# Kernel tuning notes

Measured on AMD Instinct MI355X. Metric: run time of the kernel, lower is better.

Reference implementation:

```python
import jax, jax.numpy as jnp
import numpy as np

N_NODES = 200000
N_EDGES = 600000
FP = 128


def _gru_cell(x, h, wih, whh, bih, bhh):
    # torch.nn.GRUCell: gates ordered (r, z, n)
    gi = x @ wih.T + bih
    gh = h @ whh.T + bhh
    ir, iz, inn = jnp.split(gi, 3, axis=-1)
    hr, hz, hn = jnp.split(gh, 3, axis=-1)
    r = jax.nn.sigmoid(ir + hr)
    z = jax.nn.sigmoid(iz + hz)
    n = jnp.tanh(inn + r * hn)
    return (1.0 - z) * n + z * h


def _layer(x, dst, step, aw, ab, tw, tb, wih, whh, bih, bhh):
    n_nodes = x.shape[0]
    x_i = x[dst]  # [E, F] gather of target-node features
    if step == 0:
        h_s = jnp.broadcast_to(jnp.sum(x_i, axis=-1, keepdims=True), x_i.shape)
    else:
        h_s = x_i
    esv = jax.nn.leaky_relu(jnp.concatenate([h_s, x_i], axis=-1) @ aw.T + ab)  # [E,1]
    asv = jax.nn.softmax(esv, axis=-1)  # size-1 softmax -> ones (faithful)
    cs = jax.nn.elu(asv * (h_s @ tw.T + tb))  # dropout is identity at eval
    m = _gru_cell(cs, h_s, wih, whh, bih, bhh)  # per-edge GRU update [E,F]
    return jax.ops.segment_sum(m, dst, num_segments=n_nodes)  # scatter-add aggregate


def setup_inputs() -> dict:
    key = jax.random.key(0)
    ks = jax.random.split(key, 20)
    s = 1.0 / np.sqrt(FP)
    inp = {
        "x": jax.random.normal(ks[0], (N_NODES, FP), dtype=jnp.float32),
        "edge_index": jax.random.randint(ks[1], (2, N_EDGES), 0, N_NODES, dtype=jnp.int64),
    }
    i = 2
    for l in range(2):
        inp[f"align_w{l}"] = jax.random.uniform(ks[i], (1, 2 * FP), jnp.float32, -s, s); i += 1
        inp[f"align_b{l}"] = jax.random.uniform(ks[i], (1,), jnp.float32, -s, s); i += 1
        inp[f"attend_w{l}"] = jax.random.uniform(ks[i], (FP, FP), jnp.float32, -s, s); i += 1
        inp[f"attend_b{l}"] = jax.random.uniform(ks[i], (FP,), jnp.float32, -s, s); i += 1
        inp[f"wih{l}"] = jax.random.uniform(ks[i], (3 * FP, FP), jnp.float32, -s, s); i += 1
        inp[f"whh{l}"] = jax.random.uniform(ks[i], (3 * FP, FP), jnp.float32, -s, s); i += 1
        inp[f"bih{l}"] = jax.random.uniform(ks[i], (3 * FP,), jnp.float32, -s, s); i += 1
        inp[f"bhh{l}"] = jax.random.uniform(ks[i], (3 * FP,), jnp.float32, -s, s); i += 1
    return inp


def reference(x, edge_index,
              align_w0, align_b0, attend_w0, attend_b0, wih0, whh0, bih0, bhh0,
              align_w1, align_b1, attend_w1, attend_b1, wih1, whh1, bih1, bhh1):
    dst = edge_index[1]
    x = _layer(x, dst, 0, align_w0, align_b0, attend_w0, attend_b0, wih0, whh0, bih0, bhh0)
    x = _layer(x, dst, 1, align_w1, align_b1, attend_w1, attend_b1, wih1, whh1, bih1, bhh1)
    return x
```

## Files before the change

kernel.cpp:

```cpp
#include <hip/hip_runtime.h>
#include <cmath>

#define NN 200000
#define NE 600000

typedef __bf16 bf16x8 __attribute__((ext_vector_type(8)));
typedef float f32x16 __attribute__((ext_vector_type(16)));

#define LOG2E 1.44269504088896340736f
__device__ __forceinline__ float fexp2(float x) { return __builtin_amdgcn_exp2f(x); }
__device__ __forceinline__ float frcp(float x) { return __builtin_amdgcn_rcpf(x); }
__device__ __forceinline__ float sigm(float v) { return frcp(1.0f + fexp2(-LOG2E * v)); }
__device__ __forceinline__ float ftanh(float v) {
  float t = fexp2(-2.0f * LOG2E * fabsf(v));
  float r = (1.0f - t) * frcp(1.0f + t);
  return __builtin_copysignf(r, v);
}
__device__ __forceinline__ float eluf(float v) { return v > 0.0f ? v : fexp2(LOG2E * v) - 1.0f; }

__device__ __forceinline__ unsigned short bfr(float f) {
  unsigned u = __float_as_uint(f);
  u += 0x7FFFu + ((u >> 16) & 1u);
  return (unsigned short)(u >> 16);
}
__device__ __forceinline__ void bsplit(float v, unsigned short& hi, unsigned short& lo) {
  unsigned short h = bfr(v);
  float hf = __uint_as_float(((unsigned)h) << 16);
  hi = h;
  lo = bfr(v - hf);
}


__global__ __launch_bounds__(256) void hist_kernel(const int* __restrict__ dst,
                                                   int* __restrict__ deg) {
  int e = blockIdx.x * 256 + threadIdx.x;
  if (e < NE) atomicAdd(&deg[dst[e]], 1);
}

__global__ __launch_bounds__(256) void prep_kernel(const float* __restrict__ attw0,
                                                   const float* __restrict__ whh0,
                                                   float* __restrict__ rwt0,
                                                   float* __restrict__ rwh0) {
  int gw = blockIdx.x * 4 + (threadIdx.x >> 6);
  int lane = threadIdx.x & 63;
  const float* row = (gw < 128) ? (attw0 + (size_t)gw * 128)
                                : (whh0 + (size_t)(gw - 128) * 128);
  float2 v = ((const float2*)row)[lane];
  float a = v.x + v.y;
#pragma unroll
  for (int o = 1; o < 64; o <<= 1) a += __shfl_xor(a, o, 64);
  if (lane == 0) {
    if (gw < 128) rwt0[gw] = a;
    else rwh0[gw - 128] = a;
  }
}

__global__ __launch_bounds__(256) void pack_kernel(
    const float* __restrict__ wih0, const float* __restrict__ tw1,
    const float* __restrict__ wih1, const float* __restrict__ whh1,
    unsigned short* __restrict__ w0ph, unsigned short* __restrict__ w0pl,
    unsigned short* __restrict__ w1ph, unsigned short* __restrict__ w1pl,
    unsigned short* __restrict__ w2ph, unsigned short* __restrict__ w2pl) {
  int g = blockIdx.x * 256 + threadIdx.x;
  if (g >= 20480) return;
  unsigned short *PH, *PL;
  const float* row;
  int l;
  if (g < 6144) { l = g; PH = w0ph; PL = w0pl; }
  else if (g < 8192) { l = g - 6144; PH = w1ph; PL = w1pl; }
  else { l = g - 8192; PH = w2ph; PL = w2pl; }
  int lane = l & 63, ks = (l >> 6) & 7, nt = l >> 9;
  int n = nt * 32 + (lane & 31);
  int k0 = ks * 16 + (lane >> 5) * 8;
  if (g < 6144) row = wih0 + n * 128;
  else if (g < 8192) row = tw1 + n * 128;
  else row = (n < 384) ? wih1 + n * 128 : whh1 + (n - 384) * 128;
  unsigned uh[4], ul[4];
#pragma unroll
  for (int p = 0; p < 4; p++) {
    unsigned short ah, al, bh, bl;
    bsplit(row[k0 + 2 * p], ah, al);
    bsplit(row[k0 + 2 * p + 1], bh, bl);
    uh[p] = (unsigned)ah | ((unsigned)bh << 16);
    ul[p] = (unsigned)al | ((unsigned)bl << 16);
  }
  *(uint4*)&PH[l * 8] = make_uint4(uh[0], uh[1], uh[2], uh[3]);
  *(uint4*)&PL[l * 8] = make_uint4(ul[0], ul[1], ul[2], ul[3]);
}

#define MFMA3(accv, ah, al, bh, bl)                                          \
  accv = __builtin_amdgcn_mfma_f32_32x32x16_bf16(ah, bh, accv, 0, 0, 0);     \
  accv = __builtin_amdgcn_mfma_f32_32x32x16_bf16(ah, bl, accv, 0, 0, 0);     \
  accv = __builtin_amdgcn_mfma_f32_32x32x16_bf16(al, bh, accv, 0, 0, 0);

__global__ __launch_bounds__(512, 4) void layer0_kernel(
    const float* __restrict__ x, const float* __restrict__ tb0,
    const unsigned short* __restrict__ w0ph, const unsigned short* __restrict__ w0pl,
    const float* __restrict__ bih0, const float* __restrict__ bhh0,
    const float* __restrict__ rwt0, const float* __restrict__ rwh0,
    const int* __restrict__ deg,
    unsigned short* __restrict__ x1h, unsigned short* __restrict__ x1l) {
  __shared__ float s_lds[64];
  __shared__ float deg_lds[64];
  __shared__ unsigned short csh[8192];
  __shared__ unsigned short csl[8192];

  const int tid = threadIdx.x;
  const int lane = tid & 63;
  const int wv = tid >> 6;
  const int mg = wv & 1;
  const int cb = wv >> 1;
  const int n0 = blockIdx.x * 64;

  if (tid < 64) deg_lds[tid] = (float)deg[n0 + tid];

  {
    int m = tid >> 3, c = (tid & 7) * 16;
    const float4* xr = (const float4*)(x + (size_t)(n0 + m) * 128 + c);
    float a = 0.f;
#pragma unroll
    for (int q = 0; q < 4; q++) { float4 v = xr[q]; a += v.x + v.y + v.z + v.w; }
#pragma unroll
    for (int o = 1; o < 8; o <<= 1) a += __shfl_xor(a, o, 64);
    if ((tid & 7) == 0) s_lds[m] = a;
  }
  __syncthreads();

  {
    int m = lane, c = wv;
    float s = s_lds[m];
    int kb = c * 16;
    int fb = (((m >> 5) * 8 + c) * 64 + (m & 31)) * 8;
#pragma unroll
    for (int u = 0; u < 2; u++) {
      unsigned uh[4], ul[4];
#pragma unroll
      for (int p = 0; p < 4; p++) {
        int k = kb + u * 8 + p * 2;
        unsigned short h0, l0, h1, l1;
        bsplit(eluf(fmaf(s, rwt0[k], tb0[k])), h0, l0);
        bsplit(eluf(fmaf(s, rwt0[k + 1], tb0[k + 1])), h1, l1);
        uh[p] = (unsigned)h0 | ((unsigned)h1 << 16);
        ul[p] = (unsigned)l0 | ((unsigned)l1 << 16);
      }
      *(uint4*)&csh[fb + u * 256] = make_uint4(uh[0], uh[1], uh[2], uh[3]);
      *(uint4*)&csl[fb + u * 256] = make_uint4(ul[0], ul[1], ul[2], ul[3]);
    }
  }
  __syncthreads();

  f32x16 acc[3] = {};
#pragma unroll
  for (int ks = 0; ks < 8; ks++) {
    bf16x8 ah = *(const bf16x8*)&csh[((mg * 8 + ks) * 64 + lane) * 8];
    bf16x8 al = *(const bf16x8*)&csl[((mg * 8 + ks) * 64 + lane) * 8];
#pragma unroll
    for (int g = 0; g < 3; g++) {
      int nt = g * 4 + cb;
      size_t base = (size_t)((nt * 8 + ks) * 64 + lane) * 8;
      bf16x8 bh = *(const bf16x8*)&w0ph[base];
      bf16x8 bl = *(const bf16x8*)&w0pl[base];
      MFMA3(acc[g], ah, al, bh, bl);
    }
  }

  const int jc = cb * 32 + (lane & 31);
  float bir = bih0[jc], biz = bih0[jc + 128], bin_ = bih0[jc + 256];
  float bhr = bhh0[jc], bhz = bhh0[jc + 128], bhn = bhh0[jc + 256];
  float rwr = rwh0[jc], rwz = rwh0[jc + 128], rwn = rwh0[jc + 256];
  const size_t tbase = (size_t)blockIdx.x * 8192;
  const int fj = ((mg * 8 + (cb * 2 + ((lane >> 4) & 1))) * 64 + ((lane >> 3) & 1) * 32) * 8 +
                 (lane & 7);
#pragma unroll
  for (int reg = 0; reg < 16; reg++) {
    int crow = (reg & 3) + 8 * (reg >> 2) + 4 * (lane >> 5);
    int m = mg * 32 + crow;
    float s = s_lds[m];
    float dd = deg_lds[m];
    float r = sigm(acc[0][reg] + bir + fmaf(s, rwr, bhr));
    float z = sigm(acc[1][reg] + biz + fmaf(s, rwz, bhz));
    float nn2 = ftanh(fmaf(r, fmaf(s, rwn, bhn), acc[2][reg] + bin_));
    float v = dd * ((1.f - z) * nn2 + z * s);
    unsigned short vh, vl;
    bsplit(v, vh, vl);
    unsigned pv = (unsigned)vh | ((unsigned)vl << 16);
    unsigned pu = __shfl_xor(pv, 1, 64);
    if ((lane & 1) == 0) {
      size_t f = tbase + fj + crow * 8;
      *(unsigned*)&x1h[f] = (pv & 0xFFFFu) | (pu << 16);
      *(unsigned*)&x1l[f] = (pv >> 16) | (pu & 0xFFFF0000u);
    }
  }
}

__global__ __launch_bounds__(512, 4) void layer1_kernel(
    const unsigned short* __restrict__ x1h, const unsigned short* __restrict__ x1l,
    const float* __restrict__ tb1,
    const unsigned short* __restrict__ w1ph, const unsigned short* __restrict__ w1pl,
    const unsigned short* __restrict__ w2ph, const unsigned short* __restrict__ w2pl,
    const float* __restrict__ bih1, const float* __restrict__ bhh1,
    const int* __restrict__ deg, float* __restrict__ out) {
  __shared__ unsigned short cfh[8192];
  __shared__ unsigned short cfl[8192];
  __shared__ float deg_lds[64];

  const int tid = threadIdx.x;
  const int lane = tid & 63;
  const int wv = tid >> 6;
  const int mg = wv & 1;
  const int cb = wv >> 1;
  const int n0 = blockIdx.x * 64;
  const size_t tbase = (size_t)blockIdx.x * 8192;

  if (tid < 64) deg_lds[tid] = (float)deg[n0 + tid];

  f32x16 aA[4] = {};
#pragma unroll
  for (int ks = 0; ks < 8; ks++) {
    bf16x8 ah = *(const bf16x8*)&x1h[tbase + ((mg * 8 + ks) * 64 + lane) * 8];
    bf16x8 al = *(const bf16x8*)&x1l[tbase + ((mg * 8 + ks) * 64 + lane) * 8];
    {
      size_t base = (size_t)((cb * 8 + ks) * 64 + lane) * 8;
      bf16x8 bh = *(const bf16x8*)&w1ph[base];
      bf16x8 bl = *(const bf16x8*)&w1pl[base];
      MFMA3(aA[3], ah, al, bh, bl);
    }
#pragma unroll
    for (int g = 0; g < 3; g++) {
      int nt = 12 + g * 4 + cb;
      size_t base = (size_t)((nt * 8 + ks) * 64 + lane) * 8;
      bf16x8 bh = *(const bf16x8*)&w2ph[base];
      bf16x8 bl = *(const bf16x8*)&w2pl[base];
      MFMA3(aA[g], ah, al, bh, bl);
    }
  }

  {
    float tbj = tb1[cb * 32 + (lane & 31)];
    const int fj = ((mg * 8 + (cb * 2 + ((lane >> 4) & 1))) * 64 + ((lane >> 3) & 1) * 32) * 8 +
                   (lane & 7);
#pragma unroll
    for (int reg = 0; reg < 16; reg++) {
      int crow = (reg & 3) + 8 * (reg >> 2) + 4 * (lane >> 5);
      unsigned short vh, vl;
      bsplit(eluf(aA[3][reg] + tbj), vh, vl);
      unsigned pv = (unsigned)vh | ((unsigned)vl << 16);
      unsigned pu = __shfl_xor(pv, 1, 64);
      if ((lane & 1) == 0) {
        int f = fj + crow * 8;
        *(unsigned*)&cfh[f] = (pv & 0xFFFFu) | (pu << 16);
        *(unsigned*)&cfl[f] = (pv >> 16) | (pu & 0xFFFF0000u);
      }
    }
  }
  __syncthreads();

  f32x16 aB[1] = {};
#pragma unroll
  for (int ks = 0; ks < 8; ks++) {
    bf16x8 ch = *(const bf16x8*)&cfh[((mg * 8 + ks) * 64 + lane) * 8];
    bf16x8 cl = *(const bf16x8*)&cfl[((mg * 8 + ks) * 64 + lane) * 8];
#pragma unroll
    for (int g = 0; g < 3; g++) {
      int nt = g * 4 + cb;
      size_t base = (size_t)((nt * 8 + ks) * 64 + lane) * 8;
      bf16x8 bh = *(const bf16x8*)&w2ph[base];
      bf16x8 bl = *(const bf16x8*)&w2pl[base];
      if (g == 0) { MFMA3(aA[0], ch, cl, bh, bl); }
      else if (g == 1) { MFMA3(aA[1], ch, cl, bh, bl); }
      else { MFMA3(aB[0], ch, cl, bh, bl); }
    }
  }

  const int jc = cb * 32 + (lane & 31);
  float bir = bih1[jc], biz = bih1[jc + 128], bin_ = bih1[jc + 256];
  float bhr = bhh1[jc], bhz = bhh1[jc + 128], bhn = bhh1[jc + 256];
  const int fj = ((mg * 8 + (cb * 2 + ((lane >> 4) & 1))) * 64 + ((lane >> 3) & 1) * 32) * 8 +
                 (lane & 7);
#pragma unroll
  for (int reg = 0; reg < 16; reg++) {
    int crow = (reg & 3) + 8 * (reg >> 2) + 4 * (lane >> 5);
    int m = mg * 32 + crow;
    float dd = deg_lds[m];
    float r = sigm(aA[0][reg] + bir + bhr);
    float z = sigm(aA[1][reg] + biz + bhz);
    float nn2 = ftanh(fmaf(r, aA[2][reg] + bhn, aB[0][reg] + bin_));
    size_t f = tbase + fj + crow * 8;
    float hfull = (float)(*(const __bf16*)&x1h[f]) + (float)(*(const __bf16*)&x1l[f]);
    out[(size_t)(n0 + m) * 128 + jc] = dd * ((1.f - z) * nn2 + z * hfull);
  }
}

extern "C" void kernel_launch(void* const* d_in, const int* in_sizes, int n_in,
                              void* d_out, int out_size, void* d_ws, size_t ws_size,
                              hipStream_t stream) {
  const float* x     = (const float*)d_in[0];
  const int*   edge  = (const int*)d_in[1];
  const float* attw0 = (const float*)d_in[4];
  const float* attb0 = (const float*)d_in[5];
  const float* wih0  = (const float*)d_in[6];
  const float* whh0  = (const float*)d_in[7];
  const float* bih0  = (const float*)d_in[8];
  const float* bhh0  = (const float*)d_in[9];
  const float* attw1 = (const float*)d_in[12];
  const float* attb1 = (const float*)d_in[13];
  const float* wih1  = (const float*)d_in[14];
  const float* whh1  = (const float*)d_in[15];
  const float* bih1  = (const float*)d_in[16];
  const float* bhh1  = (const float*)d_in[17];

  float* ws = (float*)d_ws;
  unsigned short* x1h = (unsigned short*)ws;
  unsigned short* x1l = (unsigned short*)(ws + 12800000);
  int*   deg  = (int*)(ws + 25600000);
  float* rwt0 = ws + 25800000;
  float* rwh0 = ws + 25800128;
  unsigned short* wp = (unsigned short*)(ws + 25800512);
  unsigned short* w0ph = wp;
  unsigned short* w0pl = wp + 49152;
  unsigned short* w1ph = wp + 98304;
  unsigned short* w1pl = wp + 114688;
  unsigned short* w2ph = wp + 131072;
  unsigned short* w2pl = wp + 229376;

  const int* dst = edge + NE;

  hipMemsetAsync(deg, 0, NN * sizeof(int), stream);
  hist_kernel<<<(NE + 255) / 256, 256, 0, stream>>>(dst, deg);
  prep_kernel<<<128, 256, 0, stream>>>(attw0, whh0, rwt0, rwh0);
  pack_kernel<<<80, 256, 0, stream>>>(wih0, attw1, wih1, whh1,
                                      w0ph, w0pl, w1ph, w1pl, w2ph, w2pl);
  layer0_kernel<<<NN / 64, 512, 0, stream>>>(x, attb0, w0ph, w0pl, bih0, bhh0,
                                             rwt0, rwh0, deg, x1h, x1l);
  layer1_kernel<<<NN / 64, 512, 0, stream>>>(x1h, x1l, attb1, w1ph, w1pl, w2ph, w2pl,
                                             bih1, bhh1, deg, (float*)d_out);
}
```

Before: 473.8 us.

## Fuse layer0 and layer1 into one kernel keeping intermediate in LDS

Merges the two per-node layer kernels into one, so the layer-0 output stays in shared memory as bf16 hi/lo split tiles instead of a global workspace round-trip. The layer-1 GEMMs are reordered to read that tile from LDS. This removes the global write and re-read of the intermediate node features and one kernel launch. In exchange, dynamic LDS use grows to 64KB per block plus extra syncs, which may lower occupancy.

```diff
diff --git a/kernel.cpp b/kernel.cpp
--- a/kernel.cpp
+++ b/kernel.cpp
@@ -93,17 +93,23 @@
   accv = __builtin_amdgcn_mfma_f32_32x32x16_bf16(ah, bl, accv, 0, 0, 0);     \
   accv = __builtin_amdgcn_mfma_f32_32x32x16_bf16(al, bh, accv, 0, 0, 0);
 
-__global__ __launch_bounds__(512, 4) void layer0_kernel(
-    const float* __restrict__ x, const float* __restrict__ tb0,
+__global__ __launch_bounds__(512, 4) void fused_kernel(
+    const float* __restrict__ x,
+    const float* __restrict__ tb0, const float* __restrict__ tb1,
     const unsigned short* __restrict__ w0ph, const unsigned short* __restrict__ w0pl,
+    const unsigned short* __restrict__ w1ph, const unsigned short* __restrict__ w1pl,
+    const unsigned short* __restrict__ w2ph, const unsigned short* __restrict__ w2pl,
     const float* __restrict__ bih0, const float* __restrict__ bhh0,
     const float* __restrict__ rwt0, const float* __restrict__ rwh0,
-    const int* __restrict__ deg,
-    unsigned short* __restrict__ x1h, unsigned short* __restrict__ x1l) {
+    const float* __restrict__ bih1, const float* __restrict__ bhh1,
+    const int* __restrict__ deg, float* __restrict__ out) {
+  extern __shared__ unsigned short smem[];
+  unsigned short* csh = smem;
+  unsigned short* csl = smem + 8192;
+  unsigned short* hfh = smem + 16384;
+  unsigned short* hfl = smem + 24576;
   __shared__ float s_lds[64];
   __shared__ float deg_lds[64];
-  __shared__ unsigned short csh[8192];
-  __shared__ unsigned short csl[8192];
 
   const int tid = threadIdx.x;
   const int lane = tid & 63;
@@ -149,7 +155,11 @@
   }
   __syncthreads();
 
-  f32x16 acc[3] = {};
+  const int jc = cb * 32 + (lane & 31);
+  const int fj = ((mg * 8 + (cb * 2 + ((lane >> 4) & 1))) * 64 + ((lane >> 3) & 1) * 32) * 8 +
+                 (lane & 7);
+
+  f32x16 g0[3] = {};
 #pragma unroll
   for (int ks = 0; ks < 8; ks++) {
     bf16x8 ah = *(const bf16x8*)&csh[((mg * 8 + ks) * 64 + lane) * 8];
@@ -160,134 +170,109 @@
       size_t base = (size_t)((nt * 8 + ks) * 64 + lane) * 8;
       bf16x8 bh = *(const bf16x8*)&w0ph[base];
       bf16x8 bl = *(const bf16x8*)&w0pl[base];
-      MFMA3(acc[g], ah, al, bh, bl);
-    }
-  }
-
-  const int jc = cb * 32 + (lane & 31);
-  float bir = bih0[jc], biz = bih0[jc + 128], bin_ = bih0[jc + 256];
-  float bhr = bhh0[jc], bhz = bhh0[jc + 128], bhn = bhh0[jc + 256];
-  float rwr = rwh0[jc], rwz = rwh0[jc + 128], rwn = rwh0[jc + 256];
-  const size_t tbase = (size_t)blockIdx.x * 8192;
-  const int fj = ((mg * 8 + (cb * 2 + ((lane >> 4) & 1))) * 64 + ((lane >> 3) & 1) * 32) * 8 +
-                 (lane & 7);
-#pragma unroll
-  for (int reg = 0; reg < 16; reg++) {
-    int crow = (reg & 3) + 8 * (reg >> 2) + 4 * (lane >> 5);
-    int m = mg * 32 + crow;
-    float s = s_lds[m];
-    float dd = deg_lds[m];
-    float r = sigm(acc[0][reg] + bir + fmaf(s, rwr, bhr));
-    float z = sigm(acc[1][reg] + biz + fmaf(s, rwz, bhz));
-    float nn2 = ftanh(fmaf(r, fmaf(s, rwn, bhn), acc[2][reg] + bin_));
-    float v = dd * ((1.f - z) * nn2 + z * s);
-    unsigned short vh, vl;
-    bsplit(v, vh, vl);
-    unsigned pv = (unsigned)vh | ((unsigned)vl << 16);
-    unsigned pu = __shfl_xor(pv, 1, 64);
-    if ((lane & 1) == 0) {
-      size_t f = tbase + fj + crow * 8;
-      *(unsigned*)&x1h[f] = (pv & 0xFFFFu) | (pu << 16);
-      *(unsigned*)&x1l[f] = (pv >> 16) | (pu & 0xFFFF0000u);
-    }
-  }
-}
-
-__global__ __launch_bounds__(512, 4) void layer1_kernel(
-    const unsigned short* __restrict__ x1h, const unsigned short* __restrict__ x1l,
-    const float* __restrict__ tb1,
-    const unsigned short* __restrict__ w1ph, const unsigned short* __restrict__ w1pl,
-    const unsigned short* __restrict__ w2ph, const unsigned short* __restrict__ w2pl,
-    const float* __restrict__ bih1, const float* __restrict__ bhh1,
-    const int* __restrict__ deg, float* __restrict__ out) {
-  __shared__ unsigned short cfh[8192];
-  __shared__ unsigned short cfl[8192];
-  __shared__ float deg_lds[64];
-
-  const int tid = threadIdx.x;
-  const int lane = tid & 63;
-  const int wv = tid >> 6;
-  const int mg = wv & 1;
-  const int cb = wv >> 1;
-  const int n0 = blockIdx.x * 64;
-  const size_t tbase = (size_t)blockIdx.x * 8192;
-
-  if (tid < 64) deg_lds[tid] = (float)deg[n0 + tid];
-
-  f32x16 aA[4] = {};
-#pragma unroll
-  for (int ks = 0; ks < 8; ks++) {
-    bf16x8 ah = *(const bf16x8*)&x1h[tbase + ((mg * 8 + ks) * 64 + lane) * 8];
-    bf16x8 al = *(const bf16x8*)&x1l[tbase + ((mg * 8 + ks) * 64 + lane) * 8];
-    {
-      size_t base = (size_t)((cb * 8 + ks) * 64 + lane) * 8;
-      bf16x8 bh = *(const bf16x8*)&w1ph[base];
-      bf16x8 bl = *(const bf16x8*)&w1pl[base];
-      MFMA3(aA[3], ah, al, bh, bl);
-    }
-#pragma unroll
-    for (int g = 0; g < 3; g++) {
-      int nt = 12 + g * 4 + cb;
-      size_t base = (size_t)((nt * 8 + ks) * 64 + lane) * 8;
-      bf16x8 bh = *(const bf16x8*)&w2ph[base];
-      bf16x8 bl = *(const bf16x8*)&w2pl[base];
-      MFMA3(aA[g], ah, al, bh, bl);
-    }
-  }
-
-  {
-    float tbj = tb1[cb * 32 + (lane & 31)];
-    const int fj = ((mg * 8 + (cb * 2 + ((lane >> 4) & 1))) * 64 + ((lane >> 3) & 1) * 32) * 8 +
-                   (lane & 7);
+      MFMA3(g0[g], ah, al, bh, bl);
+    }
+  }
+
+  {
+    float bir = bih0[jc], biz = bih0[jc + 128], bin_ = bih0[jc + 256];
+    float bhr = bhh0[jc], bhz = bhh0[jc + 128], bhn = bhh0[jc + 256];
+    float rwr = rwh0[jc], rwz = rwh0[jc + 128], rwn = rwh0[jc + 256];
 #pragma unroll
     for (int reg = 0; reg < 16; reg++) {
       int crow = (reg & 3) + 8 * (reg >> 2) + 4 * (lane >> 5);
+      int m = mg * 32 + crow;
+      float s = s_lds[m];
+      float dd = deg_lds[m];
+      float r = sigm(g0[0][reg] + bir + fmaf(s, rwr, bhr));
+      float z = sigm(g0[1][reg] + biz + fmaf(s, rwz, bhz));
+      float nn2 = ftanh(fmaf(r, fmaf(s, rwn, bhn), g0[2][reg] + bin_));
+      float v = dd * ((1.f - z) * nn2 + z * s);
       unsigned short vh, vl;
-      bsplit(eluf(aA[3][reg] + tbj), vh, vl);
+      bsplit(v, vh, vl);
       unsigned pv = (unsigned)vh | ((unsigned)vl << 16);
       unsigned pu = __shfl_xor(pv, 1, 64);
       if ((lane & 1) == 0) {
         int f = fj + crow * 8;
-        *(unsigned*)&cfh[f] = (pv & 0xFFFFu) | (pu << 16);
-        *(unsigned*)&cfl[f] = (pv >> 16) | (pu & 0xFFFF0000u);
+        *(unsigned*)&hfh[f] = (pv & 0xFFFFu) | (pu << 16);
+        *(unsigned*)&hfl[f] = (pv >> 16) | (pu & 0xFFFF0000u);
       }
     }
   }
   __syncthreads();
 
-  f32x16 aB[1] = {};
+  f32x16 a1 = {};
 #pragma unroll
   for (int ks = 0; ks < 8; ks++) {
-    bf16x8 ch = *(const bf16x8*)&cfh[((mg * 8 + ks) * 64 + lane) * 8];
-    bf16x8 cl = *(const bf16x8*)&cfl[((mg * 8 + ks) * 64 + lane) * 8];
+    bf16x8 ah = *(const bf16x8*)&hfh[((mg * 8 + ks) * 64 + lane) * 8];
+    bf16x8 al = *(const bf16x8*)&hfl[((mg * 8 + ks) * 64 + lane) * 8];
+    size_t base = (size_t)((cb * 8 + ks) * 64 + lane) * 8;
+    bf16x8 bh = *(const bf16x8*)&w1ph[base];
+    bf16x8 bl = *(const bf16x8*)&w1pl[base];
+    MFMA3(a1, ah, al, bh, bl);
+  }
+
+  {
+    float tbj = tb1[jc];
+#pragma unroll
+    for (int reg = 0; reg < 16; reg++) {
+      int crow = (reg & 3) + 8 * (reg >> 2) + 4 * (lane >> 5);
+      unsigned short vh, vl;
+      bsplit(eluf(a1[reg] + tbj), vh, vl);
+      unsigned pv = (unsigned)vh | ((unsigned)vl << 16);
+      unsigned pu = __shfl_xor(pv, 1, 64);
+      if ((lane & 1) == 0) {
+        int f = fj + crow * 8;
+        *(unsigned*)&csh[f] = (pv & 0xFFFFu) | (pu << 16);
+        *(unsigned*)&csl[f] = (pv >> 16) | (pu & 0xFFFF0000u);
+      }
+    }
+  }
+  __syncthreads();
+
+  f32x16 aR = {}, aZ = {}, aGHN = {}, aGIN = {};
+#pragma unroll
+  for (int ks = 0; ks < 8; ks++) {
+    bf16x8 xh = *(const bf16x8*)&hfh[((mg * 8 + ks) * 64 + lane) * 8];
+    bf16x8 xl = *(const bf16x8*)&hfl[((mg * 8 + ks) * 64 + lane) * 8];
+    bf16x8 ch = *(const bf16x8*)&csh[((mg * 8 + ks) * 64 + lane) * 8];
+    bf16x8 cl = *(const bf16x8*)&csl[((mg * 8 + ks) * 64 + lane) * 8];
 #pragma unroll
     for (int g = 0; g < 3; g++) {
-      int nt = g * 4 + cb;
-      size_t base = (size_t)((nt * 8 + ks) * 64 + lane) * 8;
-      bf16x8 bh = *(const bf16x8*)&w2ph[base];
-      bf16x8 bl = *(const bf16x8*)&w2pl[base];
-      if (g == 0) { MFMA3(aA[0], ch, cl, bh, bl); }
-      else if (g == 1) { MFMA3(aA[1], ch, cl, bh, bl); }
-      else { MFMA3(aB[0], ch, cl, bh, bl); }
-    }
-  }
-
-  const int jc = cb * 32 + (lane & 31);
-  float bir = bih1[jc], biz = bih1[jc + 128], bin_ = bih1[jc + 256];
-  float bhr = bhh1[jc], bhz = bhh1[jc + 128], bhn = bhh1[jc + 256];
-  const int fj = ((mg * 8 + (cb * 2 + ((lane >> 4) & 1))) * 64 + ((lane >> 3) & 1) * 32) * 8 +
-                 (lane & 7);
-#pragma unroll
-  for (int reg = 0; reg < 16; reg++) {
-    int crow = (reg & 3) + 8 * (reg >> 2) + 4 * (lane >> 5);
-    int m = mg * 32 + crow;
-    float dd = deg_lds[m];
-    float r = sigm(aA[0][reg] + bir + bhr);
-    float z = sigm(aA[1][reg] + biz + bhz);
-    float nn2 = ftanh(fmaf(r, aA[2][reg] + bhn, aB[0][reg] + bin_));
-    size_t f = tbase + fj + crow * 8;
-    float hfull = (float)(*(const __bf16*)&x1h[f]) + (float)(*(const __bf16*)&x1l[f]);
-    out[(size_t)(n0 + m) * 128 + jc] = dd * ((1.f - z) * nn2 + z * hfull);
+      {
+        size_t base = (size_t)(((12 + g * 4 + cb) * 8 + ks) * 64 + lane) * 8;
+        bf16x8 bh = *(const bf16x8*)&w2ph[base];
+        bf16x8 bl = *(const bf16x8*)&w2pl[base];
+        if (g == 0) { MFMA3(aR, xh, xl, bh, bl); }
+        else if (g == 1) { MFMA3(aZ, xh, xl, bh, bl); }
+        else { MFMA3(aGHN, xh, xl, bh, bl); }
+      }
+      {
+        size_t base = (size_t)(((g * 4 + cb) * 8 + ks) * 64 + lane) * 8;
+        bf16x8 bh = *(const bf16x8*)&w2ph[base];
+        bf16x8 bl = *(const bf16x8*)&w2pl[base];
+        if (g == 0) { MFMA3(aR, ch, cl, bh, bl); }
+        else if (g == 1) { MFMA3(aZ, ch, cl, bh, bl); }
+        else { MFMA3(aGIN, ch, cl, bh, bl); }
+      }
+    }
+  }
+
+  {
+    float bir = bih1[jc], biz = bih1[jc + 128], bin_ = bih1[jc + 256];
+    float bhr = bhh1[jc], bhz = bhh1[jc + 128], bhn = bhh1[jc + 256];
+#pragma unroll
+    for (int reg = 0; reg < 16; reg++) {
+      int crow = (reg & 3) + 8 * (reg >> 2) + 4 * (lane >> 5);
+      int m = mg * 32 + crow;
+      float dd = deg_lds[m];
+      float r = sigm(aR[reg] + bir + bhr);
+      float z = sigm(aZ[reg] + biz + bhz);
+      float nn2 = ftanh(fmaf(r, aGHN[reg] + bhn, aGIN[reg] + bin_));
+      int f = fj + crow * 8;
+      float hfull = (float)(*(const __bf16*)&hfh[f]) + (float)(*(const __bf16*)&hfl[f]);
+      out[(size_t)(n0 + m) * 128 + jc] = dd * ((1.f - z) * nn2 + z * hfull);
+    }
   }
 }
 
@@ -310,8 +295,6 @@
   const float* bhh1  = (const float*)d_in[17];
 
   float* ws = (float*)d_ws;
-  unsigned short* x1h = (unsigned short*)ws;
-  unsigned short* x1l = (unsigned short*)(ws + 12800000);
   int*   deg  = (int*)(ws + 25600000);
   float* rwt0 = ws + 25800000;
   float* rwh0 = ws + 25800128;
@@ -325,13 +308,19 @@
 
   const int* dst = edge + NE;
 
+  static bool attr_done = false;
+  if (!attr_done) {
+    hipFuncSetAttribute(reinterpret_cast<const void*>(fused_kernel),
+                        hipFuncAttributeMaxDynamicSharedMemorySize, 65536);
+    attr_done = true;
+  }
+
   hipMemsetAsync(deg, 0, NN * sizeof(int), stream);
   hist_kernel<<<(NE + 255) / 256, 256, 0, stream>>>(dst, deg);
   prep_kernel<<<128, 256, 0, stream>>>(attw0, whh0, rwt0, rwh0);
   pack_kernel<<<80, 256, 0, stream>>>(wih0, attw1, wih1, whh1,
                                       w0ph, w0pl, w1ph, w1pl, w2ph, w2pl);
-  layer0_kernel<<<NN / 64, 512, 0, stream>>>(x, attb0, w0ph, w0pl, bih0, bhh0,
-                                             rwt0, rwh0, deg, x1h, x1l);
-  layer1_kernel<<<NN / 64, 512, 0, stream>>>(x1h, x1l, attb1, w1ph, w1pl, w2ph, w2pl,
-                                             bih1, bhh1, deg, (float*)d_out);
-}
+  fused_kernel<<<NN / 64, 512, 65536, stream>>>(
+      x, attb0, attb1, w0ph, w0pl, w1ph, w1pl, w2ph, w2pl,
+      bih0, bhh0, rwt0, rwh0, bih1, bhh1, deg, (float*)d_out);
+}
```

Result: faster. 450.4 us (-4.9%).
